# Kernel tuning notes

Measured on AMD Instinct MI355X. Metric: run time of the kernel, lower is better.

Reference implementation:

```python
import jax, jax.numpy as jnp
import numpy as np

B, T, D, I, E, R = 4, 2048, 2048, 6144, 8, 32


def setup_inputs() -> dict:
    key = jax.random.key(0)
    ks = jax.random.split(key, 9)
    return {
        "x": jax.random.normal(ks[0], (B, T, D), jnp.float32),
        "router_w": jax.random.normal(ks[1], (D, E), jnp.float32) * 0.02,
        "A_gate": jax.random.normal(ks[2], (E, D, R), jnp.float32) * 0.01,
        "B_gate": jax.random.normal(ks[3], (E, R, I), jnp.float32) * 0.01,
        "A_up": jax.random.normal(ks[4], (E, D, R), jnp.float32) * 0.01,
        "B_up": jax.random.normal(ks[5], (E, R, I), jnp.float32) * 0.01,
        "W_gate": jax.random.normal(ks[6], (D, I), jnp.float32) * 0.02,
        "W_up": jax.random.normal(ks[7], (D, I), jnp.float32) * 0.02,
        "W_down": jax.random.normal(ks[8], (I, D), jnp.float32) * 0.02,
    }


def reference(x, router_w, A_gate, B_gate, A_up, B_up, W_gate, W_up, W_down):
    b, t, d = x.shape
    flat = x.reshape(b * t, d)                     # [N, D]
    # Router: top-1 expert per token (argmax matches torch argmax: first max)
    gate_logits = flat @ router_w                  # [N, E]
    idx = jnp.argmax(gate_logits, axis=-1)         # [N]
    n_exp = router_w.shape[1]

    def routed_lora(A, Bm):
        # sum_e mask_e * (x @ A_e @ B_e); loop over small static expert count
        out = jnp.zeros((flat.shape[0], Bm.shape[2]), flat.dtype)
        for e in range(n_exp):
            m = (idx == e)[:, None]
            out = out + jnp.where(m, (flat @ A[e]) @ Bm[e], 0.0)
        return out

    # ExpertLoRA forward: base gate/up + per-token-selected LoRA delta, SwiGLU, down
    gate = flat @ W_gate + routed_lora(A_gate, B_gate)   # [N, I]
    up = flat @ W_up + routed_lora(A_up, B_up)           # [N, I]
    down = (jax.nn.silu(gate) * up) @ W_down             # [N, D]
    return down.reshape(b, t, d), gate_logits
```

## Files before the change

### kernel.cpp

```cpp
#include <hip/hip_runtime.h>
#include <stdint.h>

#define N_TOK 8192
#define DDIM 2048
#define IDIM 6144
#define NEXP 8
#define RLORA 32
#define NCHUNK 64
#define CHUNK 128

typedef __attribute__((ext_vector_type(8))) short short8;
typedef __attribute__((ext_vector_type(4))) float floatx4;
typedef __attribute__((ext_vector_type(4))) unsigned short ushortx4;

__device__ __forceinline__ unsigned short f2bf(float f) {
  union { float f; unsigned u; } v; v.f = f;
  unsigned u = v.u;
  unsigned r = (u + 0x7fffu + ((u >> 16) & 1u)) >> 16;
  return (unsigned short)r;
}

__device__ __forceinline__ void gload_lds16(const void* g, void* l) {
  __builtin_amdgcn_global_load_lds(
      (const __attribute__((address_space(1))) void*)g,
      (__attribute__((address_space(3))) void*)l, 16, 0, 0);
}

__global__ __launch_bounds__(256) void router_kernel(
    const float* __restrict__ x, const float* __restrict__ rw,
    float* __restrict__ logits_out, int* __restrict__ idx) {
  int wave = threadIdx.x >> 6, lane = threadIdx.x & 63;
  int n = blockIdx.x * 4 + wave;
  const float* xr = x + (size_t)n * DDIM;
  float acc[NEXP];
#pragma unroll
  for (int e = 0; e < NEXP; e++) acc[e] = 0.f;
#pragma unroll
  for (int j = 0; j < 8; j++) {
    int d = j * 256 + lane * 4;
    floatx4 v = *(const floatx4*)(xr + d);
    const float* rwd = rw + (size_t)d * NEXP;
#pragma unroll
    for (int t = 0; t < 4; t++) {
      float xv = v[t];
      const float* rr = rwd + t * NEXP;
#pragma unroll
      for (int e = 0; e < NEXP; e++) acc[e] += xv * rr[e];
    }
  }
#pragma unroll
  for (int off = 32; off > 0; off >>= 1) {
#pragma unroll
    for (int e = 0; e < NEXP; e++) acc[e] += __shfl_xor(acc[e], off, 64);
  }
  if (lane == 0) {
    float best = acc[0]; int bi = 0;
#pragma unroll
    for (int e = 1; e < NEXP; e++)
      if (acc[e] > best) { best = acc[e]; bi = e; }
    idx[n] = bi;
#pragma unroll
    for (int e = 0; e < NEXP; e++) logits_out[(size_t)n * NEXP + e] = acc[e];
  }
}

__global__ __launch_bounds__(128) void count_kernel(
    const int* __restrict__ idx, int* __restrict__ cnt) {
  __shared__ int h[NEXP];
  if (threadIdx.x < NEXP) h[threadIdx.x] = 0;
  __syncthreads();
  int n = blockIdx.x * CHUNK + threadIdx.x;
  atomicAdd(&h[idx[n]], 1);
  __syncthreads();
  if (threadIdx.x < NEXP) cnt[blockIdx.x * NEXP + threadIdx.x] = h[threadIdx.x];
}

__global__ __launch_bounds__(64) void scan_kernel(
    const int* __restrict__ cnt, int* __restrict__ off) {
  __shared__ int tot[NEXP], base[NEXP];
  int t = threadIdx.x;
  if (t < NEXP) {
    int s = 0;
    for (int c = 0; c < NCHUNK; c++) s += cnt[c * NEXP + t];
    tot[t] = s;
  }
  __syncthreads();
  if (t == 0) {
    int run = 0;
    for (int e = 0; e < NEXP; e++) { base[e] = run; run += tot[e]; }
  }
  __syncthreads();
  if (t < NEXP) {
    int run = base[t];
    for (int c = 0; c < NCHUNK; c++) { off[c * NEXP + t] = run; run += cnt[c * NEXP + t]; }
  }
}

__global__ __launch_bounds__(64) void rank_kernel(
    const int* __restrict__ idx, const int* __restrict__ off,
    int* __restrict__ sortpos, int* __restrict__ orig, int* __restrict__ eidx) {
  if (threadIdx.x != 0) return;
  int c = blockIdx.x;
  int lc[NEXP];
#pragma unroll
  for (int e = 0; e < NEXP; e++) lc[e] = 0;
  for (int t = 0; t < CHUNK; t++) {
    int n = c * CHUNK + t;
    int e = idx[n];
    int dst = off[c * NEXP + e] + lc[e]++;
    sortpos[n] = dst;
    orig[dst] = n;
    eidx[dst] = e;
  }
}

__global__ __launch_bounds__(256) void permute_x_kernel(
    const float* __restrict__ x, const int* __restrict__ sortpos,
    unsigned short* __restrict__ xb) {
  int wave = threadIdx.x >> 6, lane = threadIdx.x & 63;
  int n = blockIdx.x * 4 + wave;
  int dst = sortpos[n];
  const float* xr = x + (size_t)n * DDIM;
  unsigned short* xbr = xb + (size_t)dst * DDIM;
#pragma unroll
  for (int j = 0; j < 8; j++) {
    int d = j * 256 + lane * 4;
    floatx4 v = *(const floatx4*)(xr + d);
    ushortx4 s;
    s[0] = f2bf(v[0]); s[1] = f2bf(v[1]); s[2] = f2bf(v[2]); s[3] = f2bf(v[3]);
    *(ushortx4*)(xbr + d) = s;
  }
}

__global__ __launch_bounds__(256) void transpose_w_kernel(
    const float* __restrict__ in, unsigned short* __restrict__ out, int Rr, int Cc) {
  __shared__ float lds[32][33];
  int r0 = blockIdx.y * 32, c0 = blockIdx.x * 32;
  int tx = threadIdx.x & 31, ty = threadIdx.x >> 5;
#pragma unroll
  for (int k = 0; k < 4; k++) {
    int r = ty + k * 8;
    lds[r][tx] = in[(size_t)(r0 + r) * Cc + c0 + tx];
  }
  __syncthreads();
#pragma unroll
  for (int k = 0; k < 4; k++) {
    int cc = ty + k * 8;
    out[(size_t)(c0 + cc) * Rr + r0 + tx] = f2bf(lds[tx][cc]);
  }
}

__global__ __launch_bounds__(256) void pack_a_kernel(
    const float* __restrict__ Ag, const float* __restrict__ Au,
    unsigned short* __restrict__ aat) {
  int o = blockIdx.x * 256 + threadIdx.x;
  int h = o >> 19;
  int oo = o & ((1 << 19) - 1);
  int c = oo >> 11, d = oo & 2047;
  int e = c >> 5, r = c & 31;
  const float* src = h ? Au : Ag;
  float v = src[(e << 16) + (d << 5) + r];
  aat[(size_t)(h * 256 + c) * DDIM + d] = f2bf(v);
}

__global__ __launch_bounds__(256) void transpose_b_kernel(
    const float* __restrict__ Bg, const float* __restrict__ Bu,
    unsigned short* __restrict__ btg, unsigned short* __restrict__ btu) {
  __shared__ float lds[32][33];
  int i0 = blockIdx.x * 32, e = blockIdx.y;
  const float* in = blockIdx.z ? Bu : Bg;
  unsigned short* out = blockIdx.z ? btu : btg;
  int tx = threadIdx.x & 31, ty = threadIdx.x >> 5;
#pragma unroll
  for (int k = 0; k < 4; k++) {
    int r = ty + k * 8;
    lds[r][tx] = in[((size_t)e * RLORA + r) * IDIM + i0 + tx];
  }
  __syncthreads();
#pragma unroll
  for (int k = 0; k < 4; k++) {
    int ii = ty + k * 8;
    out[((size_t)e * IDIM + i0 + ii) * RLORA + tx] = f2bf(lds[tx][ii]);
  }
}

__global__ __launch_bounds__(256) void gemm_tsel_kernel(
    const unsigned short* __restrict__ xb, const unsigned short* __restrict__ aat,
    const int* __restrict__ eidx, unsigned short* __restrict__ Tsel) {
  __shared__ __align__(16) unsigned short sA[4096], sB[2048];
  __shared__ int es_s[128];
  const int row0 = blockIdx.x * 128;
  const int tid = threadIdx.x;
  const int wave = tid >> 6, lane = tid & 63;
  const int wr = wave >> 1, wc = wave & 1;
  const int q = lane >> 4, m16 = lane & 15;
  if (tid < 128) es_s[tid] = eidx[row0 + tid];
  __syncthreads();
  const int emin = es_s[0], emax = es_s[127];
  int erow[4];
#pragma unroll
  for (int m = 0; m < 4; m++) erow[m] = es_s[wr * 64 + m * 16 + m16];
  floatx4 acc[8];
#pragma unroll
  for (int i = 0; i < 8; i++)
#pragma unroll
    for (int j = 0; j < 4; j++) acc[i][j] = 0.f;
  short8 zero;
#pragma unroll
  for (int i = 0; i < 8; i++) zero[i] = 0;
  for (int ee = emin; ee <= emax; ee++) {
    for (int k0 = 0; k0 < DDIM; k0 += 32) {
      __syncthreads();
#pragma unroll
      for (int rr = 0; rr < 2; rr++) {
        int e = tid * 8 + rr * 2048;
        int r = e >> 5, kk = e & 31;
        gload_lds16(xb + (size_t)(row0 + r) * DDIM + (k0 + kk), sA + e);
      }
      {
        int e2 = tid * 8;
        int c = e2 >> 5, kk = e2 & 31;
        int srow = (c < 32) ? (ee * 32 + c) : (256 + ee * 32 + (c - 32));
        gload_lds16(aat + (size_t)srow * DDIM + (k0 + kk), sB + e2);
      }
      __syncthreads();
      short8 a[4], b[2];
#pragma unroll
      for (int m = 0; m < 4; m++) {
        short8 av = *(const short8*)(sA + (wr * 64 + m * 16 + m16) * 32 + q * 8);
        a[m] = (erow[m] == ee) ? av : zero;
      }
#pragma unroll
      for (int n = 0; n < 2; n++)
        b[n] = *(const short8*)(sB + (wc * 32 + n * 16 + m16) * 32 + q * 8);
#pragma unroll
      for (int m = 0; m < 4; m++)
#pragma unroll
        for (int n = 0; n < 2; n++)
          acc[m * 2 + n] = __builtin_amdgcn_mfma_f32_16x16x32_bf16(a[m], b[n], acc[m * 2 + n], 0, 0, 0);
    }
  }
#pragma unroll
  for (int m = 0; m < 4; m++)
#pragma unroll
    for (int n = 0; n < 2; n++)
#pragma unroll
      for (int r = 0; r < 4; r++) {
        int grow = row0 + wr * 64 + m * 16 + q * 4 + r;
        int gcol = wc * 32 + n * 16 + m16;
        Tsel[(size_t)grow * 64 + gcol] = f2bf(acc[m * 2 + n][r]);
      }
}

__global__ __launch_bounds__(256, 3) void gemm_gateup_kernel(
    const unsigned short* __restrict__ xb, const unsigned short* __restrict__ wgt,
    const unsigned short* __restrict__ wut, const unsigned short* __restrict__ Tsel,
    const unsigned short* __restrict__ btg, const unsigned short* __restrict__ btu,
    const int* __restrict__ eidx, unsigned short* __restrict__ hbuf) {
  __shared__ __align__(16) unsigned short smem[12288];
  __shared__ int es_s[128];
  unsigned short* sA  = smem;
  unsigned short* sBg = smem + 4096;
  unsigned short* sBu = smem + 6144;
  unsigned short* sTg = smem;
  unsigned short* sTu = smem + 4096;
  unsigned short* sbg = smem + 8192;
  unsigned short* sbu = smem + 10240;

  floatx4 accg[8], accu[8];
#pragma unroll
  for (int i = 0; i < 8; i++)
#pragma unroll
    for (int j = 0; j < 4; j++) { accg[i][j] = 0.f; accu[i][j] = 0.f; }

  int lin = blockIdx.x;
  int xcd = lin & 7, slot = lin >> 3;
  int grp = slot >> 8, sub = slot & 255;
  int bx = xcd * 12 + grp * 4 + (sub & 3);
  int by = sub >> 2;
  const int row0 = by * 128, col0 = bx * 64;

  const int tid = threadIdx.x;
  const int wave = tid >> 6, lane = tid & 63;
  const int wr = wave >> 1, wc = wave & 1;
  const int q = lane >> 4, m16 = lane & 15;

  for (int k0 = 0; k0 < DDIM; k0 += 32) {
    __syncthreads();
#pragma unroll
    for (int rr = 0; rr < 2; rr++) {
      int e = tid * 8 + rr * 2048;
      int r = e >> 5, kk = e & 31;
      gload_lds16(xb + (size_t)(row0 + r) * DDIM + (k0 + kk), sA + e);
    }
    {
      int e2 = tid * 8;
      int c = e2 >> 5, kk = e2 & 31;
      gload_lds16(wgt + (size_t)(col0 + c) * DDIM + (k0 + kk), sBg + e2);
      gload_lds16(wut + (size_t)(col0 + c) * DDIM + (k0 + kk), sBu + e2);
    }
    __syncthreads();
    short8 a[4], bg[2], bu[2];
#pragma unroll
    for (int m = 0; m < 4; m++)
      a[m] = *(const short8*)(sA + (wr * 64 + m * 16 + m16) * 32 + q * 8);
#pragma unroll
    for (int n = 0; n < 2; n++) {
      bg[n] = *(const short8*)(sBg + (wc * 32 + n * 16 + m16) * 32 + q * 8);
      bu[n] = *(const short8*)(sBu + (wc * 32 + n * 16 + m16) * 32 + q * 8);
    }
#pragma unroll
    for (int m = 0; m < 4; m++)
#pragma unroll
      for (int n = 0; n < 2; n++) {
        accg[m * 2 + n] = __builtin_amdgcn_mfma_f32_16x16x32_bf16(a[m], bg[n], accg[m * 2 + n], 0, 0, 0);
        accu[m * 2 + n] = __builtin_amdgcn_mfma_f32_16x16x32_bf16(a[m], bu[n], accu[m * 2 + n], 0, 0, 0);
      }
  }

  __syncthreads();
  if (tid < 128) es_s[tid] = eidx[row0 + tid];
#pragma unroll
  for (int rr = 0; rr < 2; rr++) {
    int e = tid * 8 + rr * 2048;
    int r = e >> 5, kk = e & 31;
    *(floatx4*)(sTg + e) = *(const floatx4*)(Tsel + (size_t)(row0 + r) * 64 + kk);
    *(floatx4*)(sTu + e) = *(const floatx4*)(Tsel + (size_t)(row0 + r) * 64 + 32 + kk);
  }
  __syncthreads();
  const int emin = es_s[0], emax = es_s[127];
  int erow[4];
#pragma unroll
  for (int m = 0; m < 4; m++) erow[m] = es_s[wr * 64 + m * 16 + m16];
  short8 zero;
#pragma unroll
  for (int i = 0; i < 8; i++) zero[i] = 0;
  for (int ee = emin; ee <= emax; ee++) {
    __syncthreads();
    {
      int e2 = tid * 8;
      int c = e2 >> 5, kk = e2 & 31;
      *(floatx4*)(sbg + e2) = *(const floatx4*)(btg + ((size_t)ee * IDIM + col0 + c) * RLORA + kk);
      *(floatx4*)(sbu + e2) = *(const floatx4*)(btu + ((size_t)ee * IDIM + col0 + c) * RLORA + kk);
    }
    __syncthreads();
    short8 bg[2], bu[2], tg[4], tu[4];
#pragma unroll
    for (int n = 0; n < 2; n++) {
      bg[n] = *(const short8*)(sbg + (wc * 32 + n * 16 + m16) * 32 + q * 8);
      bu[n] = *(const short8*)(sbu + (wc * 32 + n * 16 + m16) * 32 + q * 8);
    }
#pragma unroll
    for (int m = 0; m < 4; m++) {
      int rloc = wr * 64 + m * 16 + m16;
      tg[m] = (erow[m] == ee) ? *(const short8*)(sTg + rloc * 32 + q * 8) : zero;
      tu[m] = (erow[m] == ee) ? *(const short8*)(sTu + rloc * 32 + q * 8) : zero;
    }
#pragma unroll
    for (int m = 0; m < 4; m++)
#pragma unroll
      for (int n = 0; n < 2; n++) {
        accg[m * 2 + n] = __builtin_amdgcn_mfma_f32_16x16x32_bf16(tg[m], bg[n], accg[m * 2 + n], 0, 0, 0);
        accu[m * 2 + n] = __builtin_amdgcn_mfma_f32_16x16x32_bf16(tu[m], bu[n], accu[m * 2 + n], 0, 0, 0);
      }
  }

#pragma unroll
  for (int m = 0; m < 4; m++)
#pragma unroll
    for (int n = 0; n < 2; n++)
#pragma unroll
      for (int r = 0; r < 4; r++) {
        int grow = row0 + wr * 64 + m * 16 + q * 4 + r;
        int gcol = col0 + wc * 32 + n * 16 + m16;
        float gv = accg[m * 2 + n][r];
        float hv = gv / (1.f + __expf(-gv)) * accu[m * 2 + n][r];
        hbuf[(size_t)grow * IDIM + gcol] = f2bf(hv);
      }
}

__device__ __forceinline__ void mm_main(const unsigned short* __restrict__ Ab,
                                        const unsigned short* __restrict__ Bb,
                                        int K, int row0, int col0,
                                        unsigned short* sA, unsigned short* sB,
                                        floatx4* acc) {
  const int tid = threadIdx.x;
  const int wave = tid >> 6, lane = tid & 63;
  const int wr = wave >> 1, wc = wave & 1;
  const int q = lane >> 4, m16 = lane & 15;
  for (int k0 = 0; k0 < K; k0 += 32) {
    __syncthreads();
#pragma unroll
    for (int rr = 0; rr < 2; rr++) {
      int e = tid * 8 + rr * 2048;
      int r = e >> 5, kk = e & 31;
      gload_lds16(Ab + (size_t)(row0 + r) * K + (k0 + kk), sA + e);
      gload_lds16(Bb + (size_t)(col0 + r) * K + (k0 + kk), sB + e);
    }
    __syncthreads();
    short8 a[4], b[4];
#pragma unroll
    for (int m = 0; m < 4; m++)
      a[m] = *(const short8*)(sA + (wr * 64 + m * 16 + m16) * 32 + q * 8);
#pragma unroll
    for (int n = 0; n < 4; n++)
      b[n] = *(const short8*)(sB + (wc * 64 + n * 16 + m16) * 32 + q * 8);
#pragma unroll
    for (int m = 0; m < 4; m++)
#pragma unroll
      for (int n = 0; n < 4; n++)
        acc[m * 4 + n] = __builtin_amdgcn_mfma_f32_16x16x32_bf16(a[m], b[n], acc[m * 4 + n], 0, 0, 0);
  }
}

__global__ __launch_bounds__(256) void gemm_down_kernel(
    const unsigned short* __restrict__ hb, const unsigned short* __restrict__ wdt,
    const int* __restrict__ orig, float* __restrict__ out) {
  __shared__ __align__(16) unsigned short sA[4096], sB[4096];
  floatx4 acc[16];
#pragma unroll
  for (int i = 0; i < 16; i++)
#pragma unroll
    for (int j = 0; j < 4; j++) acc[i][j] = 0.f;
  int lin = blockIdx.x;
  int xcd = lin & 7, slot = lin >> 3;
  int bx = xcd * 2 + (slot & 1);
  int by = slot >> 1;
  int row0 = by * 128, col0 = bx * 128;
  mm_main(hb, wdt, IDIM, row0, col0, sA, sB, acc);
  const int wave = threadIdx.x >> 6, lane = threadIdx.x & 63;
  const int wr = wave >> 1, wc = wave & 1;
  const int q = lane >> 4, m16 = lane & 15;
#pragma unroll
  for (int m = 0; m < 4; m++)
#pragma unroll
    for (int n = 0; n < 4; n++)
#pragma unroll
      for (int r = 0; r < 4; r++) {
        int grow = row0 + wr * 64 + m * 16 + q * 4 + r;
        int orow = orig[grow];
        int gcol = col0 + wc * 64 + n * 16 + m16;
        out[(size_t)orow * DDIM + gcol] = acc[m * 4 + n][r];
      }
}

extern "C" void kernel_launch(void* const* d_in, const int* in_sizes, int n_in,
                              void* d_out, int out_size, void* d_ws, size_t ws_size,
                              hipStream_t stream) {
  const float* x  = (const float*)d_in[0];
  const float* rw = (const float*)d_in[1];
  const float* Ag = (const float*)d_in[2];
  const float* Bg = (const float*)d_in[3];
  const float* Au = (const float*)d_in[4];
  const float* Bu = (const float*)d_in[5];
  const float* Wg = (const float*)d_in[6];
  const float* Wu = (const float*)d_in[7];
  const float* Wd = (const float*)d_in[8];
  float* out = (float*)d_out;
  float* logits = out + (size_t)N_TOK * DDIM;

  char* ws = (char*)d_ws;
  size_t off = 0;
  auto alloc = [&](size_t bytes) {
    char* p = ws + off;
    off += (bytes + 255) & ~(size_t)255;
    return p;
  };
  unsigned short* xb  = (unsigned short*)alloc((size_t)N_TOK * DDIM * 2);
  unsigned short* wgt = (unsigned short*)alloc((size_t)IDIM * DDIM * 2);
  unsigned short* wut = (unsigned short*)alloc((size_t)IDIM * DDIM * 2);
  unsigned short* wdt = (unsigned short*)alloc((size_t)DDIM * IDIM * 2);
  unsigned short* aat = (unsigned short*)alloc((size_t)512 * DDIM * 2);
  unsigned short* btg = (unsigned short*)alloc((size_t)NEXP * IDIM * RLORA * 2);
  unsigned short* btu = (unsigned short*)alloc((size_t)NEXP * IDIM * RLORA * 2);
  unsigned short* Tsel= (unsigned short*)alloc((size_t)N_TOK * 64 * 2);
  unsigned short* hbuf= (unsigned short*)alloc((size_t)N_TOK * IDIM * 2);
  int* idx     = (int*)alloc((size_t)N_TOK * 4);
  int* sortpos = (int*)alloc((size_t)N_TOK * 4);
  int* orig    = (int*)alloc((size_t)N_TOK * 4);
  int* eidx    = (int*)alloc((size_t)N_TOK * 4);
  int* cnt     = (int*)alloc((size_t)NCHUNK * NEXP * 4);
  int* offb    = (int*)alloc((size_t)NCHUNK * NEXP * 4);

  router_kernel<<<N_TOK / 4, 256, 0, stream>>>(x, rw, logits, idx);
  count_kernel<<<NCHUNK, 128, 0, stream>>>(idx, cnt);
  scan_kernel<<<1, 64, 0, stream>>>(cnt, offb);
  rank_kernel<<<NCHUNK, 64, 0, stream>>>(idx, offb, sortpos, orig, eidx);
  permute_x_kernel<<<N_TOK / 4, 256, 0, stream>>>(x, sortpos, xb);
  transpose_w_kernel<<<dim3(IDIM / 32, DDIM / 32), 256, 0, stream>>>(Wg, wgt, DDIM, IDIM);
  transpose_w_kernel<<<dim3(IDIM / 32, DDIM / 32), 256, 0, stream>>>(Wu, wut, DDIM, IDIM);
  transpose_w_kernel<<<dim3(DDIM / 32, IDIM / 32), 256, 0, stream>>>(Wd, wdt, IDIM, DDIM);
  pack_a_kernel<<<4096, 256, 0, stream>>>(Ag, Au, aat);
  transpose_b_kernel<<<dim3(IDIM / 32, NEXP, 2), 256, 0, stream>>>(Bg, Bu, btg, btu);
  gemm_tsel_kernel<<<N_TOK / 128, 256, 0, stream>>>(xb, aat, eidx, Tsel);
  gemm_gateup_kernel<<<(IDIM / 64) * (N_TOK / 128), 256, 0, stream>>>(
      xb, wgt, wut, Tsel, btg, btu, eidx, hbuf);
  gemm_down_kernel<<<(DDIM / 128) * (N_TOK / 128), 256, 0, stream>>>(hbuf, wdt, orig, out);
}
```

Baseline: 1.216 ms.

## Interleave gate/up weights and use 256x256 multi-stage pipelined gate-up GEMM

Gate and up weight columns are interleaved into one matrix, and the LoRA B matrices are packed into a single zero-padded K=64 block. This lets the gate-up kernel run as one 256x256-tile GEMM with 512 threads, a 4-stage LDS ring buffer with XOR swizzling, explicit vmcnt waits and MFMA priority hints. The SwiGLU epilogue pairs adjacent columns via lane shuffles. The goal is more data reuse per tile and overlap of global loads with MFMA work. The costs are 128 accumulator registers per thread, 128KB of LDS per block, and a larger padded B buffer.

```diff
diff --git a/kernel.cpp b/kernel.cpp
--- a/kernel.cpp
+++ b/kernel.cpp
@@ -147,6 +147,27 @@
   for (int k = 0; k < 4; k++) {
     int cc = ty + k * 8;
     out[(size_t)(c0 + cc) * Rr + r0 + tx] = f2bf(lds[tx][cc]);
+  }
+}
+
+__global__ __launch_bounds__(256) void transpose_wint_kernel(
+    const float* __restrict__ Wg, const float* __restrict__ Wu,
+    unsigned short* __restrict__ wint) {
+  __shared__ float lds[32][33];
+  int r0 = blockIdx.y * 32, c0 = blockIdx.x * 32;
+  const float* in = blockIdx.z ? Wu : Wg;
+  int w = blockIdx.z;
+  int tx = threadIdx.x & 31, ty = threadIdx.x >> 5;
+#pragma unroll
+  for (int k = 0; k < 4; k++) {
+    int r = ty + k * 8;
+    lds[r][tx] = in[(size_t)(r0 + r) * IDIM + c0 + tx];
+  }
+  __syncthreads();
+#pragma unroll
+  for (int k = 0; k < 4; k++) {
+    int cc = ty + k * 8;
+    wint[(size_t)(2 * (c0 + cc) + w) * DDIM + r0 + tx] = f2bf(lds[tx][cc]);
   }
 }
 
@@ -163,25 +184,25 @@
   aat[(size_t)(h * 256 + c) * DDIM + d] = f2bf(v);
 }
 
-__global__ __launch_bounds__(256) void transpose_b_kernel(
+__global__ __launch_bounds__(256) void pack_bl_kernel(
     const float* __restrict__ Bg, const float* __restrict__ Bu,
-    unsigned short* __restrict__ btg, unsigned short* __restrict__ btu) {
-  __shared__ float lds[32][33];
-  int i0 = blockIdx.x * 32, e = blockIdx.y;
-  const float* in = blockIdx.z ? Bu : Bg;
-  unsigned short* out = blockIdx.z ? btu : btg;
-  int tx = threadIdx.x & 31, ty = threadIdx.x >> 5;
-#pragma unroll
-  for (int k = 0; k < 4; k++) {
-    int r = ty + k * 8;
-    lds[r][tx] = in[((size_t)e * RLORA + r) * IDIM + i0 + tx];
-  }
-  __syncthreads();
-#pragma unroll
-  for (int k = 0; k < 4; k++) {
-    int ii = ty + k * 8;
-    out[((size_t)e * IDIM + i0 + ii) * RLORA + tx] = f2bf(lds[tx][ii]);
-  }
+    unsigned short* __restrict__ BL) {
+  int o = (blockIdx.x * 256 + threadIdx.x) * 4;
+  int kk = o & 63;
+  int t2 = o >> 6;
+  int c = t2 % (2 * IDIM);
+  int e = t2 / (2 * IDIM);
+  int j = c >> 1, w = c & 1;
+  ushortx4 s;
+#pragma unroll
+  for (int r = 0; r < 4; r++) {
+    int k = kk + r;
+    float v;
+    if (w == 0) v = (k < 32) ? Bg[((size_t)e * RLORA + k) * IDIM + j] : 0.f;
+    else        v = (k >= 32) ? Bu[((size_t)e * RLORA + (k - 32)) * IDIM + j] : 0.f;
+    s[r] = f2bf(v);
+  }
+  *(ushortx4*)(BL + o) = s;
 }
 
 __global__ __launch_bounds__(256) void gemm_tsel_kernel(
@@ -252,130 +273,173 @@
       }
 }
 
-__global__ __launch_bounds__(256, 3) void gemm_gateup_kernel(
-    const unsigned short* __restrict__ xb, const unsigned short* __restrict__ wgt,
-    const unsigned short* __restrict__ wut, const unsigned short* __restrict__ Tsel,
-    const unsigned short* __restrict__ btg, const unsigned short* __restrict__ btu,
+__global__ __launch_bounds__(512, 2) void gemm_gateup_kernel(
+    const unsigned short* __restrict__ xb, const unsigned short* __restrict__ wint,
+    const unsigned short* __restrict__ Tsel, const unsigned short* __restrict__ BL,
     const int* __restrict__ eidx, unsigned short* __restrict__ hbuf) {
-  __shared__ __align__(16) unsigned short smem[12288];
-  __shared__ int es_s[128];
-  unsigned short* sA  = smem;
-  unsigned short* sBg = smem + 4096;
-  unsigned short* sBu = smem + 6144;
-  unsigned short* sTg = smem;
-  unsigned short* sTu = smem + 4096;
-  unsigned short* sbg = smem + 8192;
-  unsigned short* sbu = smem + 10240;
-
-  floatx4 accg[8], accu[8];
-#pragma unroll
-  for (int i = 0; i < 8; i++)
-#pragma unroll
-    for (int j = 0; j < 4; j++) { accg[i][j] = 0.f; accu[i][j] = 0.f; }
+  __shared__ __align__(16) unsigned short smem[65536];
 
   int lin = blockIdx.x;
   int xcd = lin & 7, slot = lin >> 3;
-  int grp = slot >> 8, sub = slot & 255;
-  int bx = xcd * 12 + grp * 4 + (sub & 3);
-  int by = sub >> 2;
-  const int row0 = by * 128, col0 = bx * 64;
+  int grp = slot >> 6, r = slot & 63;
+  int bx = xcd * 6 + grp * 2 + (r & 1);
+  int by = r >> 1;
+  const int row0 = by * 256, col0 = bx * 256;
 
   const int tid = threadIdx.x;
-  const int wave = tid >> 6, lane = tid & 63;
-  const int wr = wave >> 1, wc = wave & 1;
+  const int lane = tid & 63, wave = tid >> 6;
+  const int wm = wave >> 2, wn = wave & 3;
   const int q = lane >> 4, m16 = lane & 15;
 
-  for (int k0 = 0; k0 < DDIM; k0 += 32) {
-    __syncthreads();
-#pragma unroll
-    for (int rr = 0; rr < 2; rr++) {
-      int e = tid * 8 + rr * 2048;
-      int r = e >> 5, kk = e & 31;
-      gload_lds16(xb + (size_t)(row0 + r) * DDIM + (k0 + kk), sA + e);
-    }
-    {
-      int e2 = tid * 8;
-      int c = e2 >> 5, kk = e2 & 31;
-      gload_lds16(wgt + (size_t)(col0 + c) * DDIM + (k0 + kk), sBg + e2);
-      gload_lds16(wut + (size_t)(col0 + c) * DDIM + (k0 + kk), sBu + e2);
-    }
-    __syncthreads();
-    short8 a[4], bg[2], bu[2];
-#pragma unroll
-    for (int m = 0; m < 4; m++)
-      a[m] = *(const short8*)(sA + (wr * 64 + m * 16 + m16) * 32 + q * 8);
-#pragma unroll
-    for (int n = 0; n < 2; n++) {
-      bg[n] = *(const short8*)(sBg + (wc * 32 + n * 16 + m16) * 32 + q * 8);
-      bu[n] = *(const short8*)(sBu + (wc * 32 + n * 16 + m16) * 32 + q * 8);
-    }
-#pragma unroll
-    for (int m = 0; m < 4; m++)
-#pragma unroll
-      for (int n = 0; n < 2; n++) {
-        accg[m * 2 + n] = __builtin_amdgcn_mfma_f32_16x16x32_bf16(a[m], bg[n], accg[m * 2 + n], 0, 0, 0);
-        accu[m * 2 + n] = __builtin_amdgcn_mfma_f32_16x16x32_bf16(a[m], bu[n], accu[m * 2 + n], 0, 0, 0);
-      }
-  }
-
-  __syncthreads();
-  if (tid < 128) es_s[tid] = eidx[row0 + tid];
-#pragma unroll
-  for (int rr = 0; rr < 2; rr++) {
-    int e = tid * 8 + rr * 2048;
-    int r = e >> 5, kk = e & 31;
-    *(floatx4*)(sTg + e) = *(const floatx4*)(Tsel + (size_t)(row0 + r) * 64 + kk);
-    *(floatx4*)(sTu + e) = *(const floatx4*)(Tsel + (size_t)(row0 + r) * 64 + 32 + kk);
-  }
-  __syncthreads();
-  const int emin = es_s[0], emax = es_s[127];
-  int erow[4];
-#pragma unroll
-  for (int m = 0; m < 4; m++) erow[m] = es_s[wr * 64 + m * 16 + m16];
+  floatx4 acc[32];
+#pragma unroll
+  for (int i = 0; i < 32; i++)
+#pragma unroll
+    for (int j = 0; j < 4; j++) acc[i][j] = 0.f;
+
+  auto stage = [&](int kt) {
+    unsigned short* Ab = smem + (kt & 3) * 16384;
+    unsigned short* Bb = Ab + 8192;
+#pragma unroll
+    for (int ch = 0; ch < 2; ch++) {
+      int o = ch * 4096 + tid * 8;
+      int rw2 = o >> 5, g = (o >> 3) & 3;
+      int gs = g ^ ((rw2 >> 1) & 3);
+      gload_lds16(xb + (size_t)(row0 + rw2) * DDIM + kt * 32 + gs * 8, Ab + o);
+    }
+#pragma unroll
+    for (int ch = 0; ch < 2; ch++) {
+      int o = ch * 4096 + tid * 8;
+      int rw2 = o >> 5, g = (o >> 3) & 3;
+      int gs = g ^ ((rw2 >> 1) & 3);
+      gload_lds16(wint + (size_t)(col0 + rw2) * DDIM + kt * 32 + gs * 8, Bb + o);
+    }
+  };
+
+  stage(0); stage(1); stage(2);
+
+  int offA[8], offB[4];
+#pragma unroll
+  for (int m = 0; m < 8; m++) {
+    int rw2 = wm * 128 + m * 16 + m16;
+    offA[m] = rw2 * 32 + ((q ^ ((rw2 >> 1) & 3)) * 8);
+  }
+#pragma unroll
+  for (int n = 0; n < 4; n++) {
+    int c = wn * 64 + n * 16 + m16;
+    offB[n] = 8192 + c * 32 + ((q ^ ((c >> 1) & 3)) * 8);
+  }
+
+  for (int kt = 0; kt < 64; kt++) {
+    if (kt < 62)      asm volatile("s_waitcnt vmcnt(8)" ::: "memory");
+    else if (kt == 62) asm volatile("s_waitcnt vmcnt(4)" ::: "memory");
+    else               asm volatile("s_waitcnt vmcnt(0)" ::: "memory");
+    __builtin_amdgcn_s_barrier();
+    __builtin_amdgcn_sched_barrier(0);
+    if (kt + 3 < 64) stage(kt + 3);
+    const unsigned short* base = smem + (kt & 3) * 16384;
+    short8 a[8], b[4];
+#pragma unroll
+    for (int m = 0; m < 8; m++) a[m] = *(const short8*)(base + offA[m]);
+#pragma unroll
+    for (int n = 0; n < 4; n++) b[n] = *(const short8*)(base + offB[n]);
+    __builtin_amdgcn_s_setprio(1);
+#pragma unroll
+    for (int m = 0; m < 8; m++)
+#pragma unroll
+      for (int n = 0; n < 4; n++)
+        acc[m * 4 + n] = __builtin_amdgcn_mfma_f32_16x16x32_bf16(a[m], b[n], acc[m * 4 + n], 0, 0, 0);
+    __builtin_amdgcn_s_setprio(0);
+  }
+
+#pragma unroll
+  for (int ch = 0; ch < 4; ch++) {
+    int o = ch * 4096 + tid * 8;
+    int rw2 = o >> 6, g = (o >> 3) & 7;
+    int gs = g ^ (rw2 & 7);
+    gload_lds16(Tsel + (size_t)(row0 + rw2) * 64 + gs * 8, smem + o);
+  }
+  int* es = (int*)(smem + 32768);
+  if (tid < 64) gload_lds16(eidx + row0 + tid * 4, (void*)(es + tid * 4));
+  asm volatile("s_waitcnt vmcnt(0)" ::: "memory");
+  __builtin_amdgcn_s_barrier();
+  __builtin_amdgcn_sched_barrier(0);
+
+  const int emin = es[0], emax = es[255];
+  int erow[8];
+#pragma unroll
+  for (int m = 0; m < 8; m++) erow[m] = es[wm * 128 + m * 16 + m16];
+
+  auto stage_bl = [&](int ee) {
+#pragma unroll
+    for (int ch = 0; ch < 4; ch++) {
+      int o = ch * 4096 + tid * 8;
+      int c = o >> 6, g = (o >> 3) & 7;
+      int gs = g ^ (c & 7);
+      gload_lds16(BL + ((size_t)ee * (2 * IDIM) + col0 + c) * 64 + gs * 8, smem + 16384 + o);
+    }
+  };
+  stage_bl(emin);
+  asm volatile("s_waitcnt vmcnt(0)" ::: "memory");
+  __builtin_amdgcn_s_barrier();
+  __builtin_amdgcn_sched_barrier(0);
+
   short8 zero;
 #pragma unroll
   for (int i = 0; i < 8; i++) zero[i] = 0;
+
   for (int ee = emin; ee <= emax; ee++) {
-    __syncthreads();
-    {
-      int e2 = tid * 8;
-      int c = e2 >> 5, kk = e2 & 31;
-      *(floatx4*)(sbg + e2) = *(const floatx4*)(btg + ((size_t)ee * IDIM + col0 + c) * RLORA + kk);
-      *(floatx4*)(sbu + e2) = *(const floatx4*)(btu + ((size_t)ee * IDIM + col0 + c) * RLORA + kk);
-    }
-    __syncthreads();
-    short8 bg[2], bu[2], tg[4], tu[4];
-#pragma unroll
-    for (int n = 0; n < 2; n++) {
-      bg[n] = *(const short8*)(sbg + (wc * 32 + n * 16 + m16) * 32 + q * 8);
-      bu[n] = *(const short8*)(sbu + (wc * 32 + n * 16 + m16) * 32 + q * 8);
-    }
-#pragma unroll
-    for (int m = 0; m < 4; m++) {
-      int rloc = wr * 64 + m * 16 + m16;
-      tg[m] = (erow[m] == ee) ? *(const short8*)(sTg + rloc * 32 + q * 8) : zero;
-      tu[m] = (erow[m] == ee) ? *(const short8*)(sTu + rloc * 32 + q * 8) : zero;
-    }
-#pragma unroll
-    for (int m = 0; m < 4; m++)
-#pragma unroll
-      for (int n = 0; n < 2; n++) {
-        accg[m * 2 + n] = __builtin_amdgcn_mfma_f32_16x16x32_bf16(tg[m], bg[n], accg[m * 2 + n], 0, 0, 0);
-        accu[m * 2 + n] = __builtin_amdgcn_mfma_f32_16x16x32_bf16(tu[m], bu[n], accu[m * 2 + n], 0, 0, 0);
-      }
-  }
-
-#pragma unroll
-  for (int m = 0; m < 4; m++)
-#pragma unroll
-    for (int n = 0; n < 2; n++)
-#pragma unroll
-      for (int r = 0; r < 4; r++) {
-        int grow = row0 + wr * 64 + m * 16 + q * 4 + r;
-        int gcol = col0 + wc * 32 + n * 16 + m16;
-        float gv = accg[m * 2 + n][r];
-        float hv = gv / (1.f + __expf(-gv)) * accu[m * 2 + n][r];
-        hbuf[(size_t)grow * IDIM + gcol] = f2bf(hv);
+    short8 bl[4][2];
+#pragma unroll
+    for (int n = 0; n < 4; n++) {
+      int c = wn * 64 + n * 16 + m16;
+#pragma unroll
+      for (int kk = 0; kk < 2; kk++) {
+        int gg = (kk * 4 + q) ^ (c & 7);
+        bl[n][kk] = *(const short8*)(smem + 16384 + c * 64 + gg * 8);
+      }
+    }
+#pragma unroll
+    for (int m = 0; m < 8; m++) {
+      int rw2 = wm * 128 + m * 16 + m16;
+      short8 tgm[2];
+#pragma unroll
+      for (int kk = 0; kk < 2; kk++) {
+        int gg = (kk * 4 + q) ^ (rw2 & 7);
+        short8 v = *(const short8*)(smem + rw2 * 64 + gg * 8);
+        tgm[kk] = (erow[m] == ee) ? v : zero;
+      }
+#pragma unroll
+      for (int n = 0; n < 4; n++)
+#pragma unroll
+        for (int kk = 0; kk < 2; kk++)
+          acc[m * 4 + n] = __builtin_amdgcn_mfma_f32_16x16x32_bf16(tgm[kk], bl[n][kk], acc[m * 4 + n], 0, 0, 0);
+    }
+    if (ee < emax) {
+      __builtin_amdgcn_s_barrier();
+      stage_bl(ee + 1);
+      asm volatile("s_waitcnt vmcnt(0)" ::: "memory");
+      __builtin_amdgcn_s_barrier();
+      __builtin_amdgcn_sched_barrier(0);
+    }
+  }
+
+#pragma unroll
+  for (int m = 0; m < 8; m++)
+#pragma unroll
+    for (int n = 0; n < 4; n++)
+#pragma unroll
+      for (int rr2 = 0; rr2 < 4; rr2++) {
+        float v = acc[m * 4 + n][rr2];
+        float p = __shfl_xor(v, 1, 64);
+        float g = (m16 & 1) ? p : v;
+        float u = (m16 & 1) ? v : p;
+        float h = g / (1.f + __expf(-g)) * u;
+        if (!(m16 & 1)) {
+          int grow = row0 + wm * 128 + m * 16 + q * 4 + rr2;
+          int gi = (col0 + wn * 64 + n * 16 + m16) >> 1;
+          hbuf[(size_t)grow * IDIM + gi] = f2bf(h);
+        }
       }
 }
 
@@ -467,12 +531,10 @@
     return p;
   };
   unsigned short* xb  = (unsigned short*)alloc((size_t)N_TOK * DDIM * 2);
-  unsigned short* wgt = (unsigned short*)alloc((size_t)IDIM * DDIM * 2);
-  unsigned short* wut = (unsigned short*)alloc((size_t)IDIM * DDIM * 2);
+  unsigned short* wint= (unsigned short*)alloc((size_t)2 * IDIM * DDIM * 2);
   unsigned short* wdt = (unsigned short*)alloc((size_t)DDIM * IDIM * 2);
   unsigned short* aat = (unsigned short*)alloc((size_t)512 * DDIM * 2);
-  unsigned short* btg = (unsigned short*)alloc((size_t)NEXP * IDIM * RLORA * 2);
-  unsigned short* btu = (unsigned short*)alloc((size_t)NEXP * IDIM * RLORA * 2);
+  unsigned short* BL  = (unsigned short*)alloc((size_t)NEXP * 2 * IDIM * 64 * 2);
   unsigned short* Tsel= (unsigned short*)alloc((size_t)N_TOK * 64 * 2);
   unsigned short* hbuf= (unsigned short*)alloc((size_t)N_TOK * IDIM * 2);
   int* idx     = (int*)alloc((size_t)N_TOK * 4);
@@ -487,13 +549,12 @@
   scan_kernel<<<1, 64, 0, stream>>>(cnt, offb);
   rank_kernel<<<NCHUNK, 64, 0, stream>>>(idx, offb, sortpos, orig, eidx);
   permute_x_kernel<<<N_TOK / 4, 256, 0, stream>>>(x, sortpos, xb);
-  transpose_w_kernel<<<dim3(IDIM / 32, DDIM / 32), 256, 0, stream>>>(Wg, wgt, DDIM, IDIM);
-  transpose_w_kernel<<<dim3(IDIM / 32, DDIM / 32), 256, 0, stream>>>(Wu, wut, DDIM, IDIM);
   transpose_w_kernel<<<dim3(DDIM / 32, IDIM / 32), 256, 0, stream>>>(Wd, wdt, IDIM, DDIM);
+  transpose_wint_kernel<<<dim3(IDIM / 32, DDIM / 32, 2), 256, 0, stream>>>(Wg, Wu, wint);
   pack_a_kernel<<<4096, 256, 0, stream>>>(Ag, Au, aat);
-  transpose_b_kernel<<<dim3(IDIM / 32, NEXP, 2), 256, 0, stream>>>(Bg, Bu, btg, btu);
+  pack_bl_kernel<<<(NEXP * 2 * IDIM * 64) / 1024, 256, 0, stream>>>(Bg, Bu, BL);
   gemm_tsel_kernel<<<N_TOK / 128, 256, 0, stream>>>(xb, aat, eidx, Tsel);
-  gemm_gateup_kernel<<<(IDIM / 64) * (N_TOK / 128), 256, 0, stream>>>(
-      xb, wgt, wut, Tsel, btg, btu, eidx, hbuf);
+  gemm_gateup_kernel<<<(N_TOK / 256) * (2 * IDIM / 256), 512, 0, stream>>>(
+      xb, wint, Tsel, BL, eidx, hbuf);
   gemm_down_kernel<<<(DDIM / 128) * (N_TOK / 128), 256, 0, stream>>>(hbuf, wdt, orig, out);
 }
```

New measurement: 1.151 ms. -5.4%, faster.
